# Optimization experiments

Hardware: AMD Instinct MI355X
Metric: run time of the kernel (lower is better)

## Reference

```python
import jax, jax.numpy as jnp
import numpy as np

N, L, S, C, H = 8, 1024, 1024, 512, 8
SCALE = float((C // H) ** 0.5)  # sqrt(64), as in source (based on embed_dim, not cat'd dim)


def _linear_params(key, c_in, c_out):
    kw, kb = jax.random.split(key)
    lim = 1.0 / np.sqrt(c_in)
    W = jax.random.uniform(kw, (c_out, c_in), jnp.float32, -lim, lim)
    b = jax.random.uniform(kb, (c_out,), jnp.float32, -lim, lim)
    return W, b


def setup_inputs() -> dict:
    key = jax.random.key(0)
    ks = jax.random.split(key, 12)
    inp = {
        'q_c': jax.random.normal(ks[0], (N, L, C), jnp.float32),
        'q_p': jax.random.normal(ks[1], (N, L, C), jnp.float32),
        'k_c': jax.random.normal(ks[2], (N, S, C), jnp.float32),
        'k_p': jax.random.normal(ks[3], (N, S, C), jnp.float32),
        'v': jax.random.normal(ks[4], (N, S, C), jnp.float32),
        'attn_mask': jax.random.normal(ks[5], (N, H, L, S), jnp.float32),
    }
    for i, name in enumerate(['qc', 'qp', 'kc', 'kp', 'v', 'o']):
        W, b = _linear_params(ks[6 + i], C, C)
        inp[f'W_{name}'] = W
        inp[f'b_{name}'] = b
    return inp


def _split_head(x, h):
    n, l, c = x.shape
    return x.reshape(n, l, h, c // h).transpose(0, 2, 1, 3)  # (N,H,L,c/h)


def reference(q_c, q_p, k_c, k_p, v, attn_mask,
              W_qc, b_qc, W_qp, b_qp, W_kc, b_kc, W_kp, b_kp, W_v, b_v, W_o, b_o):
    # dual projections + cat -> (N, L, 2C)
    q = jnp.concatenate([q_c @ W_qc.T + b_qc, q_p @ W_qp.T + b_qp], axis=-1)
    k = jnp.concatenate([k_c @ W_kc.T + b_kc, k_p @ W_kp.T + b_kp], axis=-1)
    vv = v @ W_v.T + b_v
    q = _split_head(q, H)   # (N,H,L,2C/H)
    k = _split_head(k, H)   # (N,H,S,2C/H)
    vv = _split_head(vv, H)  # (N,H,S,C/H)
    attn = jnp.einsum('nhld,nhsd->nhls', q / SCALE, k) + attn_mask
    attn = jax.nn.softmax(attn, axis=-1)
    out = jnp.einsum('nhls,nhsd->nhld', attn, vv)
    out = out.transpose(0, 2, 1, 3).reshape(N, L, C)
    return out @ W_o.T + b_o
```

## Files before the change

### kernel.cpp

```cpp
#include <hip/hip_runtime.h>
#include <hip/hip_bf16.h>

typedef __bf16 bf16;
typedef __bf16 bf16x8 __attribute__((ext_vector_type(8)));
typedef float  f32x4  __attribute__((ext_vector_type(4)));
typedef float  f32x2  __attribute__((ext_vector_type(2)));

#define LOG2E        1.4426950408889634f
#define QSCALE_LOG2E 0.18033688011112043f
#define DEFER_THR    20.0f

#define GLDS(g, l)                                                        \
  __builtin_amdgcn_global_load_lds(                                       \
      (const __attribute__((address_space(1))) void*)(g),                 \
      (__attribute__((address_space(3))) void*)(l), 16, 0, 0)

#define WAITV(n) asm volatile("s_waitcnt vmcnt(" #n ")" ::: "memory")
#define BARRIER() do {                                                    \
  __builtin_amdgcn_s_barrier();                                           \
  __builtin_amdgcn_sched_barrier(0);                                      \
} while (0)

__device__ __forceinline__ void stage_f32_tile(const float* __restrict__ src, int ld,
                                               char* dst, int tid) {
  #pragma unroll
  for (int t = 0; t < 8; ++t) {
    int c8  = tid + t * 256;
    int row = c8 >> 4;
    int h8  = c8 & 15;
    const f32x4 v = *reinterpret_cast<const f32x4*>(src + row * ld + h8 * 4);
    union { bf16 h[4]; unsigned long long u; } pk;
    pk.h[0] = (bf16)v[0]; pk.h[1] = (bf16)v[1];
    pk.h[2] = (bf16)v[2]; pk.h[3] = (bf16)v[3];
    int byte = (row << 7) + ((((h8 >> 1) ^ (row & 7)) << 4) | ((h8 & 1) << 3));
    *reinterpret_cast<unsigned long long*>(dst + byte) = pk.u;
  }
}

__device__ __forceinline__ void stage_bf16_tile(const bf16* __restrict__ src, int ld,
                                                char* dst, int tid) {
  #pragma unroll
  for (int t = 0; t < 4; ++t) {
    int c   = tid + t * 256;
    int row = c >> 3;
    int ck  = c & 7;
    const bf16x8 v = *reinterpret_cast<const bf16x8*>(src + row * ld + ck * 8);
    int byte = (row << 7) + (((ck ^ (row & 7)) << 4));
    *reinterpret_cast<bf16x8*>(dst + byte) = v;
  }
}

__global__ __launch_bounds__(256) void proj_gemm(
    const float* __restrict__ qc, const float* __restrict__ qp,
    const float* __restrict__ kc, const float* __restrict__ kp,
    const float* __restrict__ vin,
    const float* __restrict__ Wqc, const float* __restrict__ bqc,
    const float* __restrict__ Wqp, const float* __restrict__ bqp,
    const float* __restrict__ Wkc, const float* __restrict__ bkc,
    const float* __restrict__ Wkp, const float* __restrict__ bkp,
    const float* __restrict__ Wv,  const float* __restrict__ bv,
    bf16* __restrict__ Qws, bf16* __restrict__ Kws, bf16* __restrict__ Vtws) {
  __shared__ __align__(16) bf16 lA[128 * 64];
  __shared__ __align__(16) bf16 lB[128 * 64];
  char* lAb = (char*)lA;
  char* lBb = (char*)lB;

  const int bxr = blockIdx.x;
  const int bx  = (bxr & 7) * 160 + (bxr >> 3);
  const int g  = bx >> 8;
  const int mt = (bx & 255) >> 2;
  const int nt = bx & 3;

  const float *A, *W, *bias;
  if      (g == 0) { A = qc;  W = Wqc; bias = bqc; }
  else if (g == 1) { A = qp;  W = Wqp; bias = bqp; }
  else if (g == 2) { A = kc;  W = Wkc; bias = bkc; }
  else if (g == 3) { A = kp;  W = Wkp; bias = bkp; }
  else             { A = vin; W = Wv;  bias = bv;  }

  const int tid  = threadIdx.x;
  const int lane = tid & 63, wid = tid >> 6;
  const int wr = wid >> 1, wc = wid & 1;
  const int lrow = lane & 15, lgrp = lane >> 4;

  const float* Abase = A + (size_t)(mt * 128) * 512;
  const float* Wbase = W + (size_t)(nt * 128) * 512;

  const f32x4 fz = {0.f, 0.f, 0.f, 0.f};
  f32x4 acc[4][4];
  #pragma unroll
  for (int i = 0; i < 4; ++i)
    #pragma unroll
    for (int j = 0; j < 4; ++j) acc[i][j] = fz;

  for (int k0 = 0; k0 < 512; k0 += 64) {
    __syncthreads();
    stage_f32_tile(Abase + k0, 512, lAb, tid);
    stage_f32_tile(Wbase + k0, 512, lBb, tid);
    __syncthreads();
    #pragma unroll
    for (int kk = 0; kk < 2; ++kk) {
      bf16x8 af[4], bfr[4];
      #pragma unroll
      for (int mf = 0; mf < 4; ++mf) {
        int row  = wr * 64 + mf * 16 + lrow;
        int byte = (row << 7) + ((((kk << 2) | lgrp) ^ (row & 7)) << 4);
        af[mf] = *reinterpret_cast<const bf16x8*>(lAb + byte);
      }
      #pragma unroll
      for (int nf = 0; nf < 4; ++nf) {
        int row  = wc * 64 + nf * 16 + lrow;
        int byte = (row << 7) + ((((kk << 2) | lgrp) ^ (row & 7)) << 4);
        bfr[nf] = *reinterpret_cast<const bf16x8*>(lBb + byte);
      }
      #pragma unroll
      for (int mf = 0; mf < 4; ++mf)
        #pragma unroll
        for (int nf = 0; nf < 4; ++nf)
          acc[mf][nf] = __builtin_amdgcn_mfma_f32_16x16x32_bf16(
              af[mf], bfr[nf], acc[mf][nf], 0, 0, 0);
    }
  }

  float bcol[4];
  #pragma unroll
  for (int nf = 0; nf < 4; ++nf)
    bcol[nf] = bias[nt * 128 + wc * 64 + nf * 16 + lrow];

  #pragma unroll
  for (int mf = 0; mf < 4; ++mf) {
    #pragma unroll
    for (int nf = 0; nf < 4; ++nf) {
      #pragma unroll
      for (int r = 0; r < 4; ++r) {
        int grow = mt * 128 + wr * 64 + mf * 16 + lgrp * 4 + r;
        int col  = nt * 128 + wc * 64 + nf * 16 + lrow;
        float vv = acc[mf][nf][r] + bcol[nf];
        bf16 hb  = (bf16)vv;
        int n = grow >> 10, tt = grow & 1023;
        if (g < 2) {
          int j = (g << 9) + col;
          Qws[(size_t)((((n << 3) + (j >> 7)) << 10) | tt) * 128 + (j & 127)] = hb;
        } else if (g < 4) {
          int j  = ((g - 2) << 9) + col;
          int hh = j >> 7, d = j & 127;
          int dd = (((d >> 3) ^ ((tt >> 1) & 7)) << 3) | (d & 7);
          Kws[(size_t)((((n << 3) + hh) << 10) | tt) * 128 + dd] = hb;
        } else {
          int h = col >> 6, d = col & 63;
          int kt2 = tt >> 5, si = tt & 31;
          int ss = (((si >> 3) ^ ((d >> 1) & 3)) << 3) | (si & 7);
          Vtws[((size_t)((((n << 3) + h) << 5) + kt2) * 64 + d) * 32 + ss] = hb;
        }
      }
    }
  }
}

__global__ __launch_bounds__(512) void attn_fwd(
    const bf16* __restrict__ Qws, const bf16* __restrict__ Kws,
    const bf16* __restrict__ Vtws, const float* __restrict__ mask,
    bf16* __restrict__ Ows) {
  __shared__ __align__(16) char Kl[2][8192];
  __shared__ __align__(16) char Vl[2][4096];
  __shared__ __align__(16) char Ml[3][16384];
  __shared__ __align__(16) char Pl[8][1024];

  const int bxr = blockIdx.x;
  const int bx  = (bxr & 7) * 64 + (bxr >> 3);
  const int nh = bx >> 3;
  const int qt = bx & 7;
  const int tid = threadIdx.x;
  const int lane = tid & 63, wid = tid >> 6;
  const int lrow = lane & 15, lgrp = lane >> 4;
  const int q0 = qt * 128 + wid * 16;

  const bf16* Qb = Qws + ((size_t)(nh * 1024 + q0 + lrow)) * 128 + lgrp * 8;
  bf16x8 qf[4];
  #pragma unroll
  for (int kk = 0; kk < 4; ++kk)
    qf[kk] = *reinterpret_cast<const bf16x8*>(Qb + kk * 32);

  const float* Mg = mask + ((size_t)(nh * 1024) + qt * 128 + (wid & 1) * 64 +
                            (lane >> 3)) * 1024 + (lane & 7) * 4;
  const bf16* Kg = Kws + (size_t)nh * 131072 + lane * 8;
  const bf16* Vg = Vtws + (size_t)nh * 65536 + lane * 8;

  char* Pb = &Pl[wid][0];

  const f32x4 fz = {0.f, 0.f, 0.f, 0.f};
  f32x4 oacc[4];
  #pragma unroll
  for (int dt = 0; dt < 4; ++dt) oacc[dt] = fz;
  float m2[4], lsum[4];
  #pragma unroll
  for (int r = 0; r < 4; ++r) { m2[r] = 0.f; lsum[r] = 0.f; }

  auto stageM = [&](char* dst, int kt) {
    if (wid < 2) {
      char* d0 = dst + wid * 8192;
      #pragma unroll
      for (int i = 0; i < 8; ++i)
        GLDS(Mg + (size_t)i * 8192 + kt * 32, d0 + i * 1024);
    }
  };
  auto stageKV = [&](char* Kd, char* Vd, int kt) {
    if (wid == 2 || wid == 3) {
      #pragma unroll
      for (int j = 0; j < 4; ++j)
        GLDS(Kg + kt * 4096 + (wid - 2) * 2048 + j * 512,
             Kd + (wid - 2) * 4096 + j * 1024);
    } else if (wid == 4) {
      #pragma unroll
      for (int j = 0; j < 4; ++j)
        GLDS(Vg + kt * 2048 + j * 512, Vd + j * 1024);
    }
  };

  auto compute = [&](const char* Kb, const char* Vb, const char* Mb) {
    bf16x8 kf0[4], kf1[4], vf[4];
    #pragma unroll
    for (int kk = 0; kk < 4; ++kk) {
      int cb = ((((kk << 2) | lgrp) ^ (lrow & 7)) << 4);
      kf0[kk] = *reinterpret_cast<const bf16x8*>(Kb + lrow * 512 + cb);
      kf1[kk] = *reinterpret_cast<const bf16x8*>(Kb + lrow * 512 + 256 + cb);
    }
    #pragma unroll
    for (int dt = 0; dt < 4; ++dt)
      vf[dt] = *reinterpret_cast<const bf16x8*>(
          Vb + (dt * 16 + lrow) * 64 + ((lgrp ^ ((lrow >> 1) & 3)) << 4));
    f32x2 mk[4];
    #pragma unroll
    for (int r = 0; r < 4; ++r) {
      int qrow = wid * 16 + lgrp * 4 + r;
      mk[r] = *reinterpret_cast<const f32x2*>(Mb + qrow * 128 + lrow * 8);
    }

    f32x4 sc0 = fz, sc1 = fz;
    __builtin_amdgcn_s_setprio(1);
    #pragma unroll
    for (int kk = 0; kk < 4; ++kk)
      sc0 = __builtin_amdgcn_mfma_f32_16x16x32_bf16(qf[kk], kf0[kk], sc0, 0, 0, 0);
    #pragma unroll
    for (int kk = 0; kk < 4; ++kk)
      sc1 = __builtin_amdgcn_mfma_f32_16x16x32_bf16(qf[kk], kf1[kk], sc1, 0, 0, 0);
    __builtin_amdgcn_s_setprio(0);

    float a0r[4], a1r[4];
    bool ok = true;
    #pragma unroll
    for (int r = 0; r < 4; ++r) {
      a0r[r] = fmaf(sc0[r], QSCALE_LOG2E, mk[r].x * LOG2E);
      a1r[r] = fmaf(sc1[r], QSCALE_LOG2E, mk[r].y * LOG2E);
      ok &= (fmaxf(a0r[r], a1r[r]) <= m2[r] + DEFER_THR);
    }
    if (__builtin_expect(!__all(ok), 0)) {
      #pragma unroll
      for (int r = 0; r < 4; ++r) {
        float tv = fmaxf(a0r[r], a1r[r]);
        tv = fmaxf(tv, __shfl_xor(tv, 1));
        tv = fmaxf(tv, __shfl_xor(tv, 2));
        tv = fmaxf(tv, __shfl_xor(tv, 4));
        tv = fmaxf(tv, __shfl_xor(tv, 8));
        float mn = fmaxf(m2[r], tv);
        float corr = exp2f(m2[r] - mn);
        m2[r] = mn;
        lsum[r] *= corr;
        #pragma unroll
        for (int dt = 0; dt < 4; ++dt) oacc[dt][r] *= corr;
      }
    }
    #pragma unroll
    for (int r = 0; r < 4; ++r) {
      float e0 = exp2f(a0r[r] - m2[r]);
      float e1 = exp2f(a1r[r] - m2[r]);
      lsum[r] += e0 + e1;
      union { bf16 h[2]; unsigned u; } pk;
      pk.h[0] = (bf16)e0; pk.h[1] = (bf16)e1;
      int row = lgrp * 4 + r;
      int byte = row * 64 + ((((lrow >> 2) ^ (row & 3)) << 4) | ((lrow & 3) << 2));
      *reinterpret_cast<unsigned*>(Pb + byte) = pk.u;
    }
    __builtin_amdgcn_wave_barrier();
    __builtin_amdgcn_sched_barrier(0);
    bf16x8 pf = *reinterpret_cast<const bf16x8*>(
        Pb + lrow * 64 + ((lgrp ^ (lrow & 3)) << 4));

    __builtin_amdgcn_s_setprio(1);
    #pragma unroll
    for (int dt = 0; dt < 4; ++dt)
      oacc[dt] = __builtin_amdgcn_mfma_f32_16x16x32_bf16(pf, vf[dt], oacc[dt], 0, 0, 0);
    __builtin_amdgcn_s_setprio(0);
  };

  char *ka = &Kl[0][0], *kn = &Kl[1][0];
  char *va = &Vl[0][0], *vn = &Vl[1][0];
  char *m0 = &Ml[0][0], *m1 = &Ml[1][0], *m2p = &Ml[2][0];
  auto rotKV = [&]() {
    char* tp = ka; ka = kn; kn = tp;
    tp = va; va = vn; vn = tp;
  };
  auto rotM = [&]() {
    char* tp = m0; m0 = m1; m1 = m2p; m2p = tp;
  };

  stageKV(ka, va, 0);
  stageM(m0, 0);
  stageM(m1, 1);
  if (wid < 2) { WAITV(8); } else { WAITV(0); }
  BARRIER();

  for (int t = 0; t < 30; ++t) {
    stageKV(kn, vn, t + 1);
    stageM(m2p, t + 2);
    compute(ka, va, m0);
    if (wid < 2) { WAITV(8); } else { WAITV(0); }
    BARRIER();
    rotKV(); rotM();
  }
  stageKV(kn, vn, 31);
  compute(ka, va, m0);
  WAITV(0);
  BARRIER();
  rotKV(); rotM();

  compute(ka, va, m0);

  #pragma unroll
  for (int r = 0; r < 4; ++r) {
    float ss = lsum[r];
    ss += __shfl_xor(ss, 1);
    ss += __shfl_xor(ss, 2);
    ss += __shfl_xor(ss, 4);
    ss += __shfl_xor(ss, 8);
    lsum[r] = 1.0f / ss;
  }

  const int n = nh >> 3, h = nh & 7;
  bf16* Ob = Ows + ((size_t)(n * 1024 + q0 + lgrp * 4)) * 512 + h * 64 + lrow;
  #pragma unroll
  for (int dt = 0; dt < 4; ++dt)
    #pragma unroll
    for (int r = 0; r < 4; ++r)
      Ob[(size_t)r * 512 + dt * 16] = (bf16)(oacc[dt][r] * lsum[r]);
}

__global__ __launch_bounds__(256) void out_gemm(
    const bf16* __restrict__ Ows, const float* __restrict__ Wo,
    const float* __restrict__ bo, float* __restrict__ out) {
  __shared__ __align__(16) bf16 lA[128 * 64];
  __shared__ __align__(16) bf16 lB[128 * 64];
  char* lAb = (char*)lA;
  char* lBb = (char*)lB;

  const int bxr = blockIdx.x;
  const int bx  = (bxr & 7) * 32 + (bxr >> 3);
  const int mt = bx >> 2;
  const int nt = bx & 3;
  const int tid = threadIdx.x;
  const int lane = tid & 63, wid = tid >> 6;
  const int wr = wid >> 1, wc = wid & 1;
  const int lrow = lane & 15, lgrp = lane >> 4;

  const bf16*  Abase = Ows + (size_t)(mt * 128) * 512;
  const float* Wbase = Wo  + (size_t)(nt * 128) * 512;

  const f32x4 fz = {0.f, 0.f, 0.f, 0.f};
  f32x4 acc[4][4];
  #pragma unroll
  for (int i = 0; i < 4; ++i)
    #pragma unroll
    for (int j = 0; j < 4; ++j) acc[i][j] = fz;

  for (int k0 = 0; k0 < 512; k0 += 64) {
    __syncthreads();
    stage_bf16_tile(Abase + k0, 512, lAb, tid);
    stage_f32_tile(Wbase + k0, 512, lBb, tid);
    __syncthreads();
    #pragma unroll
    for (int kk = 0; kk < 2; ++kk) {
      bf16x8 af[4], bfr[4];
      #pragma unroll
      for (int mf = 0; mf < 4; ++mf) {
        int row  = wr * 64 + mf * 16 + lrow;
        int byte = (row << 7) + ((((kk << 2) | lgrp) ^ (row & 7)) << 4);
        af[mf] = *reinterpret_cast<const bf16x8*>(lAb + byte);
      }
      #pragma unroll
      for (int nf = 0; nf < 4; ++nf) {
        int row  = wc * 64 + nf * 16 + lrow;
        int byte = (row << 7) + ((((kk << 2) | lgrp) ^ (row & 7)) << 4);
        bfr[nf] = *reinterpret_cast<const bf16x8*>(lBb + byte);
      }
      #pragma unroll
      for (int mf = 0; mf < 4; ++mf)
        #pragma unroll
        for (int nf = 0; nf < 4; ++nf)
          acc[mf][nf] = __builtin_amdgcn_mfma_f32_16x16x32_bf16(
              af[mf], bfr[nf], acc[mf][nf], 0, 0, 0);
    }
  }

  float bcol[4];
  #pragma unroll
  for (int nf = 0; nf < 4; ++nf)
    bcol[nf] = bo[nt * 128 + wc * 64 + nf * 16 + lrow];

  #pragma unroll
  for (int mf = 0; mf < 4; ++mf) {
    #pragma unroll
    for (int nf = 0; nf < 4; ++nf) {
      #pragma unroll
      for (int r = 0; r < 4; ++r) {
        int grow = mt * 128 + wr * 64 + mf * 16 + lgrp * 4 + r;
        int col  = nt * 128 + wc * 64 + nf * 16 + lrow;
        out[(size_t)grow * 512 + col] = acc[mf][nf][r] + bcol[nf];
      }
    }
  }
}

extern "C" void kernel_launch(void* const* d_in, const int* in_sizes, int n_in,
                              void* d_out, int out_size, void* d_ws, size_t ws_size,
                              hipStream_t stream) {
  const float* qc   = (const float*)d_in[0];
  const float* qp   = (const float*)d_in[1];
  const float* kc   = (const float*)d_in[2];
  const float* kp   = (const float*)d_in[3];
  const float* vin  = (const float*)d_in[4];
  const float* mask = (const float*)d_in[5];
  const float* Wqc  = (const float*)d_in[6];
  const float* bqc  = (const float*)d_in[7];
  const float* Wqp  = (const float*)d_in[8];
  const float* bqp  = (const float*)d_in[9];
  const float* Wkc  = (const float*)d_in[10];
  const float* bkc  = (const float*)d_in[11];
  const float* Wkp  = (const float*)d_in[12];
  const float* bkp  = (const float*)d_in[13];
  const float* Wv   = (const float*)d_in[14];
  const float* bv   = (const float*)d_in[15];
  const float* Wo   = (const float*)d_in[16];
  const float* bo   = (const float*)d_in[17];

  bf16* Qws  = (bf16*)d_ws;
  bf16* Kws  = Qws  + (size_t)8 * 1024 * 1024;
  bf16* Vtws = Kws  + (size_t)8 * 1024 * 1024;
  bf16* Ows  = Vtws + (size_t)4 * 1024 * 1024;

  proj_gemm<<<dim3(1280), dim3(256), 0, stream>>>(
      qc, qp, kc, kp, vin, Wqc, bqc, Wqp, bqp, Wkc, bkc, Wkp, bkp, Wv, bv,
      Qws, Kws, Vtws);
  attn_fwd<<<dim3(512), dim3(512), 0, stream>>>(Qws, Kws, Vtws, mask, Ows);
  out_gemm<<<dim3(256), dim3(256), 0, stream>>>(Ows, Wo, bo, (float*)d_out);
}
```

Measured before the change: 185.5 us.

## Give each attention wave two 16-row query tiles to reuse K/V fragments

The attention kernel drops from 8 waves to 4 waves per block, and each wave now handles 32 query rows as two 16-row sub-tiles. K and V fragments read from LDS are reused across both sub-tiles, which halves LDS reads of K/V per unit of work and gives each wave more independent MFMA chains. Staging is rebalanced so one wave loads K and one loads V. The cost is higher register pressure and fewer waves available to hide latency.

After: 179.9 us. -3.0%, faster.

```diff
diff --git a/kernel.cpp b/kernel.cpp
--- a/kernel.cpp
+++ b/kernel.cpp
@@ -157,14 +157,14 @@
   }
 }
 
-__global__ __launch_bounds__(512) void attn_fwd(
+__global__ __launch_bounds__(256) void attn_fwd(
     const bf16* __restrict__ Qws, const bf16* __restrict__ Kws,
     const bf16* __restrict__ Vtws, const float* __restrict__ mask,
     bf16* __restrict__ Ows) {
   __shared__ __align__(16) char Kl[2][8192];
   __shared__ __align__(16) char Vl[2][4096];
   __shared__ __align__(16) char Ml[3][16384];
-  __shared__ __align__(16) char Pl[8][1024];
+  __shared__ __align__(16) char Pl[4][2048];
 
   const int bxr = blockIdx.x;
   const int bx  = (bxr & 7) * 64 + (bxr >> 3);
@@ -173,13 +173,16 @@
   const int tid = threadIdx.x;
   const int lane = tid & 63, wid = tid >> 6;
   const int lrow = lane & 15, lgrp = lane >> 4;
-  const int q0 = qt * 128 + wid * 16;
-
-  const bf16* Qb = Qws + ((size_t)(nh * 1024 + q0 + lrow)) * 128 + lgrp * 8;
-  bf16x8 qf[4];
-  #pragma unroll
-  for (int kk = 0; kk < 4; ++kk)
-    qf[kk] = *reinterpret_cast<const bf16x8*>(Qb + kk * 32);
+  const int q0 = qt * 128 + wid * 32;
+
+  bf16x8 qf[2][4];
+  #pragma unroll
+  for (int qi = 0; qi < 2; ++qi) {
+    const bf16* Qb = Qws + ((size_t)(nh * 1024 + q0 + qi * 16 + lrow)) * 128 + lgrp * 8;
+    #pragma unroll
+    for (int kk = 0; kk < 4; ++kk)
+      qf[qi][kk] = *reinterpret_cast<const bf16x8*>(Qb + kk * 32);
+  }
 
   const float* Mg = mask + ((size_t)(nh * 1024) + qt * 128 + (wid & 1) * 64 +
                             (lane >> 3)) * 1024 + (lane & 7) * 4;
@@ -189,12 +192,15 @@
   char* Pb = &Pl[wid][0];
 
   const f32x4 fz = {0.f, 0.f, 0.f, 0.f};
-  f32x4 oacc[4];
-  #pragma unroll
-  for (int dt = 0; dt < 4; ++dt) oacc[dt] = fz;
-  float m2[4], lsum[4];
-  #pragma unroll
-  for (int r = 0; r < 4; ++r) { m2[r] = 0.f; lsum[r] = 0.f; }
+  f32x4 oacc[2][4];
+  float m2[2][4], lsum[2][4];
+  #pragma unroll
+  for (int qi = 0; qi < 2; ++qi) {
+    #pragma unroll
+    for (int dt = 0; dt < 4; ++dt) oacc[qi][dt] = fz;
+    #pragma unroll
+    for (int r = 0; r < 4; ++r) { m2[qi][r] = 0.f; lsum[qi][r] = 0.f; }
+  }
 
   auto stageM = [&](char* dst, int kt) {
     if (wid < 2) {
@@ -205,12 +211,11 @@
     }
   };
   auto stageKV = [&](char* Kd, char* Vd, int kt) {
-    if (wid == 2 || wid == 3) {
-      #pragma unroll
-      for (int j = 0; j < 4; ++j)
-        GLDS(Kg + kt * 4096 + (wid - 2) * 2048 + j * 512,
-             Kd + (wid - 2) * 4096 + j * 1024);
-    } else if (wid == 4) {
+    if (wid == 2) {
+      #pragma unroll
+      for (int j = 0; j < 8; ++j)
+        GLDS(Kg + kt * 4096 + j * 512, Kd + j * 1024);
+    } else if (wid == 3) {
       #pragma unroll
       for (int j = 0; j < 4; ++j)
         GLDS(Vg + kt * 2048 + j * 512, Vd + j * 1024);
@@ -229,67 +234,85 @@
     for (int dt = 0; dt < 4; ++dt)
       vf[dt] = *reinterpret_cast<const bf16x8*>(
           Vb + (dt * 16 + lrow) * 64 + ((lgrp ^ ((lrow >> 1) & 3)) << 4));
-    f32x2 mk[4];
-    #pragma unroll
-    for (int r = 0; r < 4; ++r) {
-      int qrow = wid * 16 + lgrp * 4 + r;
-      mk[r] = *reinterpret_cast<const f32x2*>(Mb + qrow * 128 + lrow * 8);
-    }
-
-    f32x4 sc0 = fz, sc1 = fz;
+    f32x2 mk[2][4];
+    #pragma unroll
+    for (int qi = 0; qi < 2; ++qi)
+      #pragma unroll
+      for (int r = 0; r < 4; ++r) {
+        int qrow = wid * 32 + qi * 16 + lgrp * 4 + r;
+        mk[qi][r] = *reinterpret_cast<const f32x2*>(Mb + qrow * 128 + lrow * 8);
+      }
+
+    f32x4 sc0[2], sc1[2];
     __builtin_amdgcn_s_setprio(1);
     #pragma unroll
-    for (int kk = 0; kk < 4; ++kk)
-      sc0 = __builtin_amdgcn_mfma_f32_16x16x32_bf16(qf[kk], kf0[kk], sc0, 0, 0, 0);
-    #pragma unroll
-    for (int kk = 0; kk < 4; ++kk)
-      sc1 = __builtin_amdgcn_mfma_f32_16x16x32_bf16(qf[kk], kf1[kk], sc1, 0, 0, 0);
+    for (int qi = 0; qi < 2; ++qi) {
+      sc0[qi] = fz; sc1[qi] = fz;
+      #pragma unroll
+      for (int kk = 0; kk < 4; ++kk) {
+        sc0[qi] = __builtin_amdgcn_mfma_f32_16x16x32_bf16(qf[qi][kk], kf0[kk], sc0[qi], 0, 0, 0);
+        sc1[qi] = __builtin_amdgcn_mfma_f32_16x16x32_bf16(qf[qi][kk], kf1[kk], sc1[qi], 0, 0, 0);
+      }
+    }
     __builtin_amdgcn_s_setprio(0);
 
-    float a0r[4], a1r[4];
+    float a0r[2][4], a1r[2][4];
     bool ok = true;
     #pragma unroll
-    for (int r = 0; r < 4; ++r) {
-      a0r[r] = fmaf(sc0[r], QSCALE_LOG2E, mk[r].x * LOG2E);
-      a1r[r] = fmaf(sc1[r], QSCALE_LOG2E, mk[r].y * LOG2E);
-      ok &= (fmaxf(a0r[r], a1r[r]) <= m2[r] + DEFER_THR);
-    }
+    for (int qi = 0; qi < 2; ++qi)
+      #pragma unroll
+      for (int r = 0; r < 4; ++r) {
+        a0r[qi][r] = fmaf(sc0[qi][r], QSCALE_LOG2E, mk[qi][r].x * LOG2E);
+        a1r[qi][r] = fmaf(sc1[qi][r], QSCALE_LOG2E, mk[qi][r].y * LOG2E);
+        ok &= (fmaxf(a0r[qi][r], a1r[qi][r]) <= m2[qi][r] + DEFER_THR);
+      }
     if (__builtin_expect(!__all(ok), 0)) {
       #pragma unroll
+      for (int qi = 0; qi < 2; ++qi)
+        #pragma unroll
+        for (int r = 0; r < 4; ++r) {
+          float tv = fmaxf(a0r[qi][r], a1r[qi][r]);
+          tv = fmaxf(tv, __shfl_xor(tv, 1));
+          tv = fmaxf(tv, __shfl_xor(tv, 2));
+          tv = fmaxf(tv, __shfl_xor(tv, 4));
+          tv = fmaxf(tv, __shfl_xor(tv, 8));
+          float mn = fmaxf(m2[qi][r], tv);
+          float corr = exp2f(m2[qi][r] - mn);
+          m2[qi][r] = mn;
+          lsum[qi][r] *= corr;
+          #pragma unroll
+          for (int dt = 0; dt < 4; ++dt) oacc[qi][dt][r] *= corr;
+        }
+    }
+    #pragma unroll
+    for (int qi = 0; qi < 2; ++qi)
+      #pragma unroll
       for (int r = 0; r < 4; ++r) {
-        float tv = fmaxf(a0r[r], a1r[r]);
-        tv = fmaxf(tv, __shfl_xor(tv, 1));
-        tv = fmaxf(tv, __shfl_xor(tv, 2));
-        tv = fmaxf(tv, __shfl_xor(tv, 4));
-        tv = fmaxf(tv, __shfl_xor(tv, 8));
-        float mn = fmaxf(m2[r], tv);
-        float corr = exp2f(m2[r] - mn);
-        m2[r] = mn;
-        lsum[r] *= corr;
-        #pragma unroll
-        for (int dt = 0; dt < 4; ++dt) oacc[dt][r] *= corr;
-      }
-    }
-    #pragma unroll
-    for (int r = 0; r < 4; ++r) {
-      float e0 = exp2f(a0r[r] - m2[r]);
-      float e1 = exp2f(a1r[r] - m2[r]);
-      lsum[r] += e0 + e1;
-      union { bf16 h[2]; unsigned u; } pk;
-      pk.h[0] = (bf16)e0; pk.h[1] = (bf16)e1;
-      int row = lgrp * 4 + r;
-      int byte = row * 64 + ((((lrow >> 2) ^ (row & 3)) << 4) | ((lrow & 3) << 2));
-      *reinterpret_cast<unsigned*>(Pb + byte) = pk.u;
-    }
+        float e0 = exp2f(a0r[qi][r] - m2[qi][r]);
+        float e1 = exp2f(a1r[qi][r] - m2[qi][r]);
+        lsum[qi][r] += e0 + e1;
+        union { bf16 h[2]; unsigned u; } pk;
+        pk.h[0] = (bf16)e0; pk.h[1] = (bf16)e1;
+        int row = lgrp * 4 + r;
+        int byte = (qi << 10) + row * 64 +
+                   ((((lrow >> 2) ^ (row & 3)) << 4) | ((lrow & 3) << 2));
+        *reinterpret_cast<unsigned*>(Pb + byte) = pk.u;
+      }
     __builtin_amdgcn_wave_barrier();
     __builtin_amdgcn_sched_barrier(0);
-    bf16x8 pf = *reinterpret_cast<const bf16x8*>(
-        Pb + lrow * 64 + ((lgrp ^ (lrow & 3)) << 4));
+    bf16x8 pf[2];
+    #pragma unroll
+    for (int qi = 0; qi < 2; ++qi)
+      pf[qi] = *reinterpret_cast<const bf16x8*>(
+          Pb + (qi << 10) + lrow * 64 + ((lgrp ^ (lrow & 3)) << 4));
 
     __builtin_amdgcn_s_setprio(1);
     #pragma unroll
-    for (int dt = 0; dt < 4; ++dt)
-      oacc[dt] = __builtin_amdgcn_mfma_f32_16x16x32_bf16(pf, vf[dt], oacc[dt], 0, 0, 0);
+    for (int qi = 0; qi < 2; ++qi)
+      #pragma unroll
+      for (int dt = 0; dt < 4; ++dt)
+        oacc[qi][dt] = __builtin_amdgcn_mfma_f32_16x16x32_bf16(
+            pf[qi], vf[dt], oacc[qi][dt], 0, 0, 0);
     __builtin_amdgcn_s_setprio(0);
   };
 
@@ -327,22 +350,28 @@
   compute(ka, va, m0);
 
   #pragma unroll
-  for (int r = 0; r < 4; ++r) {
-    float ss = lsum[r];
-    ss += __shfl_xor(ss, 1);
-    ss += __shfl_xor(ss, 2);
-    ss += __shfl_xor(ss, 4);
-    ss += __shfl_xor(ss, 8);
-    lsum[r] = 1.0f / ss;
-  }
+  for (int qi = 0; qi < 2; ++qi)
+    #pragma unroll
+    for (int r = 0; r < 4; ++r) {
+      float ss = lsum[qi][r];
+      ss += __shfl_xor(ss, 1);
+      ss += __shfl_xor(ss, 2);
+      ss += __shfl_xor(ss, 4);
+      ss += __shfl_xor(ss, 8);
+      lsum[qi][r] = 1.0f / ss;
+    }
 
   const int n = nh >> 3, h = nh & 7;
-  bf16* Ob = Ows + ((size_t)(n * 1024 + q0 + lgrp * 4)) * 512 + h * 64 + lrow;
-  #pragma unroll
-  for (int dt = 0; dt < 4; ++dt)
-    #pragma unroll
-    for (int r = 0; r < 4; ++r)
-      Ob[(size_t)r * 512 + dt * 16] = (bf16)(oacc[dt][r] * lsum[r]);
+  #pragma unroll
+  for (int qi = 0; qi < 2; ++qi) {
+    bf16* Ob = Ows + ((size_t)(n * 1024 + q0 + qi * 16 + lgrp * 4)) * 512 +
+               h * 64 + lrow;
+    #pragma unroll
+    for (int dt = 0; dt < 4; ++dt)
+      #pragma unroll
+      for (int r = 0; r < 4; ++r)
+        Ob[(size_t)r * 512 + dt * 16] = (bf16)(oacc[qi][dt][r] * lsum[qi][r]);
+  }
 }
 
 __global__ __launch_bounds__(256) void out_gemm(
@@ -450,6 +479,6 @@
   proj_gemm<<<dim3(1280), dim3(256), 0, stream>>>(
       qc, qp, kc, kp, vin, Wqc, bqc, Wqp, bqp, Wkc, bkc, Wkp, bkp, Wv, bv,
       Qws, Kws, Vtws);
-  attn_fwd<<<dim3(512), dim3(512), 0, stream>>>(Qws, Kws, Vtws, mask, Ows);
+  attn_fwd<<<dim3(512), dim3(256), 0, stream>>>(Qws, Kws, Vtws, mask, Ows);
   out_gemm<<<dim3(256), dim3(256), 0, stream>>>(Ows, Wo, bo, (float*)d_out);
 }
```
